# Performance work log

Measured on AMD Instinct MI355X. Metric: run time of the kernel, lower is better.

The kernel has to match this reference:

```python
import jax, jax.numpy as jnp
import numpy as np
import math

B, S, D, H = 4, 1024, 1024, 16
DK = D // H


def setup_inputs() -> dict:
    key = jax.random.key(0)
    ks = jax.random.split(key, 12)
    inp = {
        "q": jax.random.normal(ks[0], (B, S, D), jnp.float32),
        "k": jax.random.normal(ks[1], (B, S, D), jnp.float32),
        "v": jax.random.normal(ks[2], (B, S, D), jnp.float32),
        # causal mask, broadcast over batch (0 = masked)
        "mask": jnp.broadcast_to(jnp.tril(jnp.ones((S, S), jnp.int32)), (B, S, S)),
    }
    sc = 1.0 / math.sqrt(D)
    # torch nn.Linear convention: y = x @ W.T + b, W:[out,in]
    inp["Wq"] = jax.random.normal(ks[3], (D, D), jnp.float32) * sc
    inp["bq"] = jnp.zeros((D,), jnp.float32)
    inp["Wk"] = jax.random.normal(ks[4], (D, D), jnp.float32) * sc
    inp["bk"] = jnp.zeros((D,), jnp.float32)
    inp["Wv"] = jax.random.normal(ks[5], (D, D), jnp.float32) * sc
    inp["bv"] = jnp.zeros((D,), jnp.float32)
    inp["Wo"] = jax.random.normal(ks[6], (D, D), jnp.float32) * sc
    inp["bo"] = jnp.zeros((D,), jnp.float32)
    return inp


def _mha(q, k, v, mask, Wq, bq, Wk, bk, Wv, bv, Wo, bo):
    def split_heads(x):  # [B,S,D] -> [B,H,S,DK]
        return x.reshape(B, S, H, DK).transpose(0, 2, 1, 3)

    qh = split_heads(q @ Wq.T + bq)
    kh = split_heads(k @ Wk.T + bk)
    vh = split_heads(v @ Wv.T + bv)

    scores = jnp.einsum("bhqd,bhkd->bhqk", qh, kh) / math.sqrt(DK)
    scores = jnp.where(mask[:, None, :, :] == 0, jnp.float32(-1e9), scores)
    weights = jax.nn.softmax(scores, axis=-1)  # dropout in eval mode -> identity
    out = jnp.einsum("bhqk,bhkd->bhqd", weights, vh)
    out = out.transpose(0, 2, 1, 3).reshape(B, S, D)
    return out @ Wo.T + bo


def reference(q, k, v, mask, Wq, bq, Wk, bk, Wv, bv, Wo, bo):
    return _mha(q, k, v, mask, Wq, bq, Wk, bk, Wv, bv, Wo, bo)
```

## Files before the change

kernel.cpp:

```cpp
#include <hip/hip_runtime.h>

typedef unsigned short u16;
typedef __bf16 bf16x8 __attribute__((ext_vector_type(8)));
typedef float floatx4 __attribute__((ext_vector_type(4)));

#define BB 4
#define SS 1024
#define DD 1024
#define HH 16
#define DKK 64
#define MM (BB*SS)

__device__ __forceinline__ u16 f2bf(float f) {
    union { float f; unsigned int u; } v; v.f = f;
    unsigned int r = v.u + 0x7fffu + ((v.u >> 16) & 1u);
    return (u16)(r >> 16);
}

__device__ __forceinline__ void async16(const u16* g, u16* l) {
    __builtin_amdgcn_global_load_lds(
        (const __attribute__((address_space(1))) void*)g,
        (__attribute__((address_space(3))) void*)l,
        16, 0, 0);
}

__global__ __launch_bounds__(256) void convert_kernel(
    const float* __restrict__ q, const float* __restrict__ k, const float* __restrict__ v,
    const float* __restrict__ Wq, const float* __restrict__ Wk, const float* __restrict__ Wv,
    const float* __restrict__ Wo,
    u16* qb, u16* kb, u16* vb, u16* Wqb, u16* Wkb, u16* Wvb, u16* Wob) {
    const int Q4 = (BB*SS*DD) / 4;
    const int W4 = (DD*DD) / 4;
    int idx = blockIdx.x * 256 + threadIdx.x;
    const float* src; u16* dst; int off;
    if (idx < Q4)            { src = q; dst = qb; off = idx; }
    else if (idx < 2*Q4)     { src = k; dst = kb; off = idx - Q4; }
    else if (idx < 3*Q4)     { src = v; dst = vb; off = idx - 2*Q4; }
    else {
        int r = idx - 3*Q4;
        int wsel = r / W4; off = r - wsel*W4;
        src = wsel==0 ? Wq : wsel==1 ? Wk : wsel==2 ? Wv : Wo;
        dst = wsel==0 ? Wqb : wsel==1 ? Wkb : wsel==2 ? Wvb : Wob;
    }
    float4 x = ((const float4*)src)[off];
    ushort4 y;
    y.x = f2bf(x.x); y.y = f2bf(x.y); y.z = f2bf(x.z); y.w = f2bf(x.w);
    ((ushort4*)dst)[off] = y;
}

__global__ __launch_bounds__(256) void qkv_gemm(
    const u16* __restrict__ qb, const u16* __restrict__ kb, const u16* __restrict__ vb,
    const u16* __restrict__ Wqb, const u16* __restrict__ Wkb, const u16* __restrict__ Wvb,
    const float* __restrict__ bq, const float* __restrict__ bk, const float* __restrict__ bv,
    u16* Qh, u16* Kh, u16* Vt) {
    const int K = DD;
    __shared__ u16 sA[128*32];
    __shared__ u16 sW[128*32];

    int flat = blockIdx.x + 24 * blockIdx.y;
    int qg  = flat >> 6;
    int rem = flat & 63;
    int nB  = rem >> 3;
    int x8  = rem & 7;
    int wmi = (qg << 3) | x8;
    int which = wmi >> 5;
    int m0 = (wmi & 31) * 128;
    int n0 = nB * 128;

    const u16* A   = which==0 ? qb  : which==1 ? kb  : vb;
    const u16* W   = which==0 ? Wqb : which==1 ? Wkb : Wvb;
    const float* bias = which==0 ? bq : which==1 ? bk : bv;
    u16* Out = which==0 ? Qh : which==1 ? Kh : Vt;
    float scale = which==0 ? 0.125f : 1.0f;

    int t = threadIdx.x;
    int w = t >> 6, l = t & 63, g = l >> 4, c = l & 15;
    int wm = w & 1, wn = w >> 1;
    int sw = (g ^ (c & 3)) * 8;

    floatx4 acc[4][4] = {};

    int srow = t >> 2;
    int sseg = (t & 3) ^ (srow & 3);
    const u16* gA0 = A + (size_t)(m0 + srow) * K + sseg*8;
    const u16* gW0 = W + (size_t)(n0 + srow) * K + sseg*8;
    u16* lA = &sA[t*8];
    u16* lW = &sW[t*8];

    for (int kk = 0; kk < K; kk += 32) {
        __syncthreads();
        async16(gA0 + kk,          lA);
        async16(gA0 + 64*K + kk,   lA + 64*32);
        async16(gW0 + kk,          lW);
        async16(gW0 + 64*K + kk,   lW + 64*32);
        __syncthreads();
        bf16x8 af[4], bf_[4];
        #pragma unroll
        for (int i = 0; i < 4; i++) af[i]  = *(const bf16x8*)&sA[(wm*64 + i*16 + c)*32 + sw];
        #pragma unroll
        for (int j = 0; j < 4; j++) bf_[j] = *(const bf16x8*)&sW[(wn*64 + j*16 + c)*32 + sw];
        #pragma unroll
        for (int i = 0; i < 4; i++)
            #pragma unroll
            for (int j = 0; j < 4; j++)
                acc[i][j] = __builtin_amdgcn_mfma_f32_16x16x32_bf16(af[i], bf_[j], acc[i][j], 0, 0, 0);
    }

    #pragma unroll
    for (int j = 0; j < 4; j++) {
        int col = n0 + wn*64 + j*16 + c;
        float bb = bias[col];
        int h = col >> 6, dk = col & 63;
        #pragma unroll
        for (int i = 0; i < 4; i++) {
            #pragma unroll
            for (int r = 0; r < 4; r++) {
                int row = m0 + wm*64 + i*16 + g*4 + r;
                int b = row >> 10, s = row & 1023;
                float vv = (acc[i][j][r] + bb) * scale;
                u16 bits = f2bf(vv);
                if (which == 2) {
                    Out[((size_t)((b*HH + h)*DKK + dk))*SS + s] = bits;
                } else {
                    Out[((size_t)(b*HH + h)*SS + s)*DKK + dk] = bits;
                }
            }
        }
    }
}

__global__ __launch_bounds__(256) void attn_kernel(
    const u16* __restrict__ Qh, const u16* __restrict__ Kh, const u16* __restrict__ Vt,
    u16* __restrict__ attnO) {
    __shared__ u16 sQ[64*64];
    __shared__ u16 sK[2][64*64];
    __shared__ u16 sVt[2][64*64];
    __shared__ u16 sP[64*72];

    int bh = blockIdx.y;
    const u16* Qp  = Qh + (size_t)bh * SS * DKK;
    const u16* Kp  = Kh + (size_t)bh * SS * DKK;
    const u16* Vtp = Vt + (size_t)bh * DKK * SS;
    int b = bh >> 4, h = bh & 15;

    int t = threadIdx.x, w = t >> 6, l = t & 63, g = l >> 4, c = l & 15;
    int wq = w * 16;
    int cx = c & 7;

    bf16x8 bones;
    {
        __bf16 one = (__bf16)1.0f, zero = (__bf16)0.0f;
        __bf16 val = (c == 0) ? one : zero;
        #pragma unroll
        for (int j = 0; j < 8; j++) bones[j] = val;
    }

    int qi0 = t, qi1 = t + 256;
    int r0 = qi0 >> 3, s0 = (qi0 & 7) ^ (r0 & 7);
    int r1 = qi1 >> 3, s1 = (qi1 & 7) ^ (r1 & 7);

    #pragma unroll
    for (int phase = 0; phase < 2; phase++) {
        int qt = phase == 0 ? (15 - (int)blockIdx.x) : (int)blockIdx.x;
        int q0 = qt * 64;

        __syncthreads();
        async16(&Qp[(q0 + r0)*DKK + s0*8], &sQ[qi0*8]);
        async16(&Qp[(q0 + r1)*DKK + s1*8], &sQ[qi1*8]);
        async16(&Kp[(r0)*DKK + s0*8],      &sK[0][qi0*8]);
        async16(&Kp[(r1)*DKK + s1*8],      &sK[0][qi1*8]);
        async16(&Vtp[r0*SS + s0*8],        &sVt[0][qi0*8]);
        async16(&Vtp[r1*SS + s1*8],        &sVt[0][qi1*8]);

        floatx4 o[4] = {};
        floatx4 ol = {};
        int cur = 0;

        for (int k0 = 0; k0 <= q0; k0 += 64) {
            __syncthreads();
            int kn = k0 + 64;
            if (kn <= q0) {
                async16(&Kp[(kn + r0)*DKK + s0*8], &sK[cur^1][qi0*8]);
                async16(&Kp[(kn + r1)*DKK + s1*8], &sK[cur^1][qi1*8]);
                async16(&Vtp[r0*SS + kn + s0*8],   &sVt[cur^1][qi0*8]);
                async16(&Vtp[r1*SS + kn + s1*8],   &sVt[cur^1][qi1*8]);
            }

            floatx4 sc_[4] = {};
            #pragma unroll
            for (int ks = 0; ks < 2; ks++) {
                int so = ((ks*4 + g) ^ cx) * 8;
                bf16x8 aq = *(const bf16x8*)&sQ[(wq + c)*64 + so];
                #pragma unroll
                for (int nt = 0; nt < 4; nt++) {
                    bf16x8 bk_ = *(const bf16x8*)&sK[cur][(nt*16 + c)*64 + so];
                    sc_[nt] = __builtin_amdgcn_mfma_f32_16x16x32_bf16(aq, bk_, sc_[nt], 0, 0, 0);
                }
            }

            if (k0 == q0) {
                #pragma unroll
                for (int nt = 0; nt < 4; nt++)
                    #pragma unroll
                    for (int r = 0; r < 4; r++) {
                        int qg = wq + g*4 + r;
                        int kg = nt*16 + c;
                        if (kg > qg) sc_[nt][r] = -1e30f;
                    }
            }

            #pragma unroll
            for (int r = 0; r < 4; r++) {
                int prow = (wq + g*4 + r)*72;
                #pragma unroll
                for (int nt = 0; nt < 4; nt++) {
                    float p = __expf(sc_[nt][r]);
                    sP[prow + nt*16 + c] = f2bf(p);
                }
            }

            #pragma unroll
            for (int ks = 0; ks < 2; ks++) {
                int so = ((ks*4 + g) ^ cx) * 8;
                bf16x8 ap = *(const bf16x8*)&sP[(wq + c)*72 + ks*32 + g*8];
                #pragma unroll
                for (int nt = 0; nt < 4; nt++) {
                    bf16x8 bv_ = *(const bf16x8*)&sVt[cur][(nt*16 + c)*64 + so];
                    o[nt] = __builtin_amdgcn_mfma_f32_16x16x32_bf16(ap, bv_, o[nt], 0, 0, 0);
                }
                ol = __builtin_amdgcn_mfma_f32_16x16x32_bf16(ap, bones, ol, 0, 0, 0);
            }
            cur ^= 1;
        }

        #pragma unroll
        for (int r = 0; r < 4; r++) {
            float lv = __shfl(ol[r], l & 48);
            float inv = 1.0f / lv;
            int row = q0 + wq + g*4 + r;
            #pragma unroll
            for (int nt = 0; nt < 4; nt++) {
                int dcol = h*64 + nt*16 + c;
                attnO[((size_t)b*SS + row)*DD + dcol] = f2bf(o[nt][r] * inv);
            }
        }
    }
}

__global__ __launch_bounds__(256) void out_gemm(
    const u16* __restrict__ A, const u16* __restrict__ W,
    const float* __restrict__ bo, float* __restrict__ out) {
    const int K = DD;
    __shared__ u16 sA[64*32];
    __shared__ u16 sW[128*32];
    int n0 = blockIdx.x * 128;
    int m0 = blockIdx.y * 64;

    int t = threadIdx.x;
    int w = t >> 6, l = t & 63, g = l >> 4, c = l & 15;
    int wm = w & 1, wn = w >> 1;
    int sw = (g ^ (c & 3)) * 8;

    floatx4 acc[2][4] = {};

    int srow = t >> 2;
    int sseg = (t & 3) ^ (srow & 3);
    const u16* gA0 = A + (size_t)(m0 + srow) * K + sseg*8;
    const u16* gW0 = W + (size_t)(n0 + srow) * K + sseg*8;
    u16* lA = &sA[t*8];
    u16* lW = &sW[t*8];

    for (int kk = 0; kk < K; kk += 32) {
        __syncthreads();
        async16(gA0 + kk,        lA);
        async16(gW0 + kk,        lW);
        async16(gW0 + 64*K + kk, lW + 64*32);
        __syncthreads();
        bf16x8 af[2], bf_[4];
        #pragma unroll
        for (int i = 0; i < 2; i++) af[i]  = *(const bf16x8*)&sA[(wm*32 + i*16 + c)*32 + sw];
        #pragma unroll
        for (int j = 0; j < 4; j++) bf_[j] = *(const bf16x8*)&sW[(wn*64 + j*16 + c)*32 + sw];
        #pragma unroll
        for (int i = 0; i < 2; i++)
            #pragma unroll
            for (int j = 0; j < 4; j++)
                acc[i][j] = __builtin_amdgcn_mfma_f32_16x16x32_bf16(af[i], bf_[j], acc[i][j], 0, 0, 0);
    }

    #pragma unroll
    for (int j = 0; j < 4; j++) {
        int col = n0 + wn*64 + j*16 + c;
        float bb = bo[col];
        #pragma unroll
        for (int i = 0; i < 2; i++) {
            #pragma unroll
            for (int r = 0; r < 4; r++) {
                int row = m0 + wm*32 + i*16 + g*4 + r;
                out[(size_t)row*DD + col] = acc[i][j][r] + bb;
            }
        }
    }
}

extern "C" void kernel_launch(void* const* d_in, const int* in_sizes, int n_in,
                              void* d_out, int out_size, void* d_ws, size_t ws_size,
                              hipStream_t stream) {
    const float* q    = (const float*)d_in[0];
    const float* k    = (const float*)d_in[1];
    const float* v    = (const float*)d_in[2];
    const float* Wq   = (const float*)d_in[4];
    const float* bq   = (const float*)d_in[5];
    const float* Wk   = (const float*)d_in[6];
    const float* bk   = (const float*)d_in[7];
    const float* Wv   = (const float*)d_in[8];
    const float* bv   = (const float*)d_in[9];
    const float* Wo   = (const float*)d_in[10];
    const float* bo   = (const float*)d_in[11];
    float* out = (float*)d_out;

    char* ws = (char*)d_ws;
    const size_t MB = 1024*1024;
    u16* qb   = (u16*)(ws + 0*MB);
    u16* kb   = (u16*)(ws + 8*MB);
    u16* vb   = (u16*)(ws + 16*MB);
    u16* Wqb  = (u16*)(ws + 24*MB);
    u16* Wkb  = (u16*)(ws + 26*MB);
    u16* Wvb  = (u16*)(ws + 28*MB);
    u16* Wob  = (u16*)(ws + 30*MB);
    u16* Qh   = (u16*)(ws + 32*MB);
    u16* Kh   = (u16*)(ws + 40*MB);
    u16* Vt   = (u16*)(ws + 48*MB);
    u16* attn = (u16*)(ws + 56*MB);

    convert_kernel<<<16384, 256, 0, stream>>>(q, k, v, Wq, Wk, Wv, Wo,
                                              qb, kb, vb, Wqb, Wkb, Wvb, Wob);
    qkv_gemm<<<dim3(24, 32), 256, 0, stream>>>(qb, kb, vb, Wqb, Wkb, Wvb,
                                               bq, bk, bv, Qh, Kh, Vt);
    attn_kernel<<<dim3(8, 64), 256, 0, stream>>>(Qh, Kh, Vt, attn);
    out_gemm<<<dim3(8, 64), 256, 0, stream>>>(attn, Wob, bo, out);
}
```

Before: 217.3 us.

## Double-buffer LDS tiles in QKV and output GEMMs and refine swizzle

Both projection GEMMs now keep two LDS buffers and issue the async global-to-LDS loads for the next K-slice before the MFMAs on the current slice. This drops one barrier per iteration and lets the global loads overlap with the matrix math. The LDS swizzle also XORs in one more row bit, to spread the fragment reads over more banks. In exchange, LDS use per block doubles, which may lower occupancy, and the end-of-iteration barrier still waits for the prefetch to finish.

```diff
diff --git a/kernel.cpp b/kernel.cpp
--- a/kernel.cpp
+++ b/kernel.cpp
@@ -54,8 +54,8 @@
     const float* __restrict__ bq, const float* __restrict__ bk, const float* __restrict__ bv,
     u16* Qh, u16* Kh, u16* Vt) {
     const int K = DD;
-    __shared__ u16 sA[128*32];
-    __shared__ u16 sW[128*32];
+    __shared__ u16 sA[2][128*32];
+    __shared__ u16 sW[2][128*32];
 
     int flat = blockIdx.x + 24 * blockIdx.y;
     int qg  = flat >> 6;
@@ -76,34 +76,42 @@
     int t = threadIdx.x;
     int w = t >> 6, l = t & 63, g = l >> 4, c = l & 15;
     int wm = w & 1, wn = w >> 1;
-    int sw = (g ^ (c & 3)) * 8;
+    int sw = (g ^ (c & 3) ^ ((c >> 2) & 1)) * 8;
 
     floatx4 acc[4][4] = {};
 
     int srow = t >> 2;
-    int sseg = (t & 3) ^ (srow & 3);
+    int sseg = (t & 3) ^ (srow & 3) ^ ((srow >> 2) & 1);
     const u16* gA0 = A + (size_t)(m0 + srow) * K + sseg*8;
     const u16* gW0 = W + (size_t)(n0 + srow) * K + sseg*8;
-    u16* lA = &sA[t*8];
-    u16* lW = &sW[t*8];
-
+
+    async16(gA0,          &sA[0][t*8]);
+    async16(gA0 + 64*K,   &sA[0][64*32 + t*8]);
+    async16(gW0,          &sW[0][t*8]);
+    async16(gW0 + 64*K,   &sW[0][64*32 + t*8]);
+    __syncthreads();
+
+    int cur = 0;
     for (int kk = 0; kk < K; kk += 32) {
-        __syncthreads();
-        async16(gA0 + kk,          lA);
-        async16(gA0 + 64*K + kk,   lA + 64*32);
-        async16(gW0 + kk,          lW);
-        async16(gW0 + 64*K + kk,   lW + 64*32);
-        __syncthreads();
+        int nxt = kk + 32;
+        if (nxt < K) {
+            async16(gA0 + nxt,        &sA[cur^1][t*8]);
+            async16(gA0 + 64*K + nxt, &sA[cur^1][64*32 + t*8]);
+            async16(gW0 + nxt,        &sW[cur^1][t*8]);
+            async16(gW0 + 64*K + nxt, &sW[cur^1][64*32 + t*8]);
+        }
         bf16x8 af[4], bf_[4];
         #pragma unroll
-        for (int i = 0; i < 4; i++) af[i]  = *(const bf16x8*)&sA[(wm*64 + i*16 + c)*32 + sw];
-        #pragma unroll
-        for (int j = 0; j < 4; j++) bf_[j] = *(const bf16x8*)&sW[(wn*64 + j*16 + c)*32 + sw];
+        for (int i = 0; i < 4; i++) af[i]  = *(const bf16x8*)&sA[cur][(wm*64 + i*16 + c)*32 + sw];
+        #pragma unroll
+        for (int j = 0; j < 4; j++) bf_[j] = *(const bf16x8*)&sW[cur][(wn*64 + j*16 + c)*32 + sw];
         #pragma unroll
         for (int i = 0; i < 4; i++)
             #pragma unroll
             for (int j = 0; j < 4; j++)
                 acc[i][j] = __builtin_amdgcn_mfma_f32_16x16x32_bf16(af[i], bf_[j], acc[i][j], 0, 0, 0);
+        __syncthreads();
+        cur ^= 1;
     }
 
     #pragma unroll
@@ -251,41 +259,48 @@
     const u16* __restrict__ A, const u16* __restrict__ W,
     const float* __restrict__ bo, float* __restrict__ out) {
     const int K = DD;
-    __shared__ u16 sA[64*32];
-    __shared__ u16 sW[128*32];
+    __shared__ u16 sA[2][64*32];
+    __shared__ u16 sW[2][128*32];
     int n0 = blockIdx.x * 128;
     int m0 = blockIdx.y * 64;
 
     int t = threadIdx.x;
     int w = t >> 6, l = t & 63, g = l >> 4, c = l & 15;
     int wm = w & 1, wn = w >> 1;
-    int sw = (g ^ (c & 3)) * 8;
+    int sw = (g ^ (c & 3) ^ ((c >> 2) & 1)) * 8;
 
     floatx4 acc[2][4] = {};
 
     int srow = t >> 2;
-    int sseg = (t & 3) ^ (srow & 3);
+    int sseg = (t & 3) ^ (srow & 3) ^ ((srow >> 2) & 1);
     const u16* gA0 = A + (size_t)(m0 + srow) * K + sseg*8;
     const u16* gW0 = W + (size_t)(n0 + srow) * K + sseg*8;
-    u16* lA = &sA[t*8];
-    u16* lW = &sW[t*8];
-
+
+    async16(gA0,          &sA[0][t*8]);
+    async16(gW0,          &sW[0][t*8]);
+    async16(gW0 + 64*K,   &sW[0][64*32 + t*8]);
+    __syncthreads();
+
+    int cur = 0;
     for (int kk = 0; kk < K; kk += 32) {
-        __syncthreads();
-        async16(gA0 + kk,        lA);
-        async16(gW0 + kk,        lW);
-        async16(gW0 + 64*K + kk, lW + 64*32);
-        __syncthreads();
+        int nxt = kk + 32;
+        if (nxt < K) {
+            async16(gA0 + nxt,        &sA[cur^1][t*8]);
+            async16(gW0 + nxt,        &sW[cur^1][t*8]);
+            async16(gW0 + 64*K + nxt, &sW[cur^1][64*32 + t*8]);
+        }
         bf16x8 af[2], bf_[4];
         #pragma unroll
-        for (int i = 0; i < 2; i++) af[i]  = *(const bf16x8*)&sA[(wm*32 + i*16 + c)*32 + sw];
-        #pragma unroll
-        for (int j = 0; j < 4; j++) bf_[j] = *(const bf16x8*)&sW[(wn*64 + j*16 + c)*32 + sw];
+        for (int i = 0; i < 2; i++) af[i]  = *(const bf16x8*)&sA[cur][(wm*32 + i*16 + c)*32 + sw];
+        #pragma unroll
+        for (int j = 0; j < 4; j++) bf_[j] = *(const bf16x8*)&sW[cur][(wn*64 + j*16 + c)*32 + sw];
         #pragma unroll
         for (int i = 0; i < 2; i++)
             #pragma unroll
             for (int j = 0; j < 4; j++)
                 acc[i][j] = __builtin_amdgcn_mfma_f32_16x16x32_bf16(af[i], bf_[j], acc[i][j], 0, 0, 0);
+        __syncthreads();
+        cur ^= 1;
     }
 
     #pragma unroll
```

After: 226.4 us. 4.2% more time.

## Fuse fp32-to-bf16 activation conversion into QKV GEMM tile loads

Applied to the files above, without the earlier changes.

Stops converting the q/k/v activations to bf16 in a separate pass and has the QKV GEMM load fp32 tiles straight into LDS, converting to bf16 when building MFMA fragments. The separate pass read 48MB of fp32 and wrote 24MB of bf16 that the GEMM then read back, so this removes that round trip; only the weight conversion remains as its own kernel. In exchange the GEMM moves twice the bytes per A tile, uses more LDS, and does the conversion in the inner loop, repeated across every N-block that reuses the same rows.

```diff
diff --git a/kernel.cpp b/kernel.cpp
--- a/kernel.cpp
+++ b/kernel.cpp
@@ -17,7 +17,7 @@
     return (u16)(r >> 16);
 }
 
-__device__ __forceinline__ void async16(const u16* g, u16* l) {
+__device__ __forceinline__ void async16(const void* g, void* l) {
     __builtin_amdgcn_global_load_lds(
         (const __attribute__((address_space(1))) void*)g,
         (__attribute__((address_space(3))) void*)l,
@@ -25,23 +25,15 @@
 }
 
 __global__ __launch_bounds__(256) void convert_kernel(
-    const float* __restrict__ q, const float* __restrict__ k, const float* __restrict__ v,
     const float* __restrict__ Wq, const float* __restrict__ Wk, const float* __restrict__ Wv,
     const float* __restrict__ Wo,
-    u16* qb, u16* kb, u16* vb, u16* Wqb, u16* Wkb, u16* Wvb, u16* Wob) {
-    const int Q4 = (BB*SS*DD) / 4;
+    u16* Wqb, u16* Wkb, u16* Wvb, u16* Wob) {
     const int W4 = (DD*DD) / 4;
     int idx = blockIdx.x * 256 + threadIdx.x;
-    const float* src; u16* dst; int off;
-    if (idx < Q4)            { src = q; dst = qb; off = idx; }
-    else if (idx < 2*Q4)     { src = k; dst = kb; off = idx - Q4; }
-    else if (idx < 3*Q4)     { src = v; dst = vb; off = idx - 2*Q4; }
-    else {
-        int r = idx - 3*Q4;
-        int wsel = r / W4; off = r - wsel*W4;
-        src = wsel==0 ? Wq : wsel==1 ? Wk : wsel==2 ? Wv : Wo;
-        dst = wsel==0 ? Wqb : wsel==1 ? Wkb : wsel==2 ? Wvb : Wob;
-    }
+    int wsel = idx / W4;
+    int off  = idx - wsel*W4;
+    const float* src = wsel==0 ? Wq : wsel==1 ? Wk : wsel==2 ? Wv : Wo;
+    u16*         dst = wsel==0 ? Wqb : wsel==1 ? Wkb : wsel==2 ? Wvb : Wob;
     float4 x = ((const float4*)src)[off];
     ushort4 y;
     y.x = f2bf(x.x); y.y = f2bf(x.y); y.z = f2bf(x.z); y.w = f2bf(x.w);
@@ -49,13 +41,13 @@
 }
 
 __global__ __launch_bounds__(256) void qkv_gemm(
-    const u16* __restrict__ qb, const u16* __restrict__ kb, const u16* __restrict__ vb,
+    const float* __restrict__ qf, const float* __restrict__ kf, const float* __restrict__ vf,
     const u16* __restrict__ Wqb, const u16* __restrict__ Wkb, const u16* __restrict__ Wvb,
     const float* __restrict__ bq, const float* __restrict__ bk, const float* __restrict__ bv,
     u16* Qh, u16* Kh, u16* Vt) {
     const int K = DD;
-    __shared__ u16 sA[128*32];
-    __shared__ u16 sW[128*32];
+    __shared__ float sAf[128*32];
+    __shared__ u16   sW[128*32];
 
     int flat = blockIdx.x + 24 * blockIdx.y;
     int qg  = flat >> 6;
@@ -67,8 +59,8 @@
     int m0 = (wmi & 31) * 128;
     int n0 = nB * 128;
 
-    const u16* A   = which==0 ? qb  : which==1 ? kb  : vb;
-    const u16* W   = which==0 ? Wqb : which==1 ? Wkb : Wvb;
+    const float* A   = which==0 ? qf  : which==1 ? kf  : vf;
+    const u16*   W   = which==0 ? Wqb : which==1 ? Wkb : Wvb;
     const float* bias = which==0 ? bq : which==1 ? bk : bv;
     u16* Out = which==0 ? Qh : which==1 ? Kh : Vt;
     float scale = which==0 ? 0.125f : 1.0f;
@@ -77,26 +69,42 @@
     int w = t >> 6, l = t & 63, g = l >> 4, c = l & 15;
     int wm = w & 1, wn = w >> 1;
     int sw = (g ^ (c & 3)) * 8;
+    int s7 = c & 7;
 
     floatx4 acc[4][4] = {};
 
+    const float* gAf[4]; float* lAf[4];
+    #pragma unroll
+    for (int qld = 0; qld < 4; qld++) {
+        int id = qld*256 + t;
+        int row = id >> 3, pq = id & 7;
+        int lq = pq ^ (row & 7);
+        gAf[qld] = A + (size_t)(m0 + row) * K + lq*4;
+        lAf[qld] = &sAf[id*4];
+    }
     int srow = t >> 2;
     int sseg = (t & 3) ^ (srow & 3);
-    const u16* gA0 = A + (size_t)(m0 + srow) * K + sseg*8;
     const u16* gW0 = W + (size_t)(n0 + srow) * K + sseg*8;
-    u16* lA = &sA[t*8];
     u16* lW = &sW[t*8];
 
     for (int kk = 0; kk < K; kk += 32) {
         __syncthreads();
-        async16(gA0 + kk,          lA);
-        async16(gA0 + 64*K + kk,   lA + 64*32);
-        async16(gW0 + kk,          lW);
-        async16(gW0 + 64*K + kk,   lW + 64*32);
+        #pragma unroll
+        for (int qld = 0; qld < 4; qld++) async16(gAf[qld] + kk, lAf[qld]);
+        async16(gW0 + kk,        lW);
+        async16(gW0 + 64*K + kk, lW + 64*32);
         __syncthreads();
         bf16x8 af[4], bf_[4];
         #pragma unroll
-        for (int i = 0; i < 4; i++) af[i]  = *(const bf16x8*)&sA[(wm*64 + i*16 + c)*32 + sw];
+        for (int i = 0; i < 4; i++) {
+            int row = wm*64 + i*16 + c;
+            const float4 lo = *(const float4*)&sAf[row*32 + (((2*g)  ) ^ s7)*4];
+            const float4 hi = *(const float4*)&sAf[row*32 + (((2*g)|1) ^ s7)*4];
+            af[i][0] = (__bf16)lo.x; af[i][1] = (__bf16)lo.y;
+            af[i][2] = (__bf16)lo.z; af[i][3] = (__bf16)lo.w;
+            af[i][4] = (__bf16)hi.x; af[i][5] = (__bf16)hi.y;
+            af[i][6] = (__bf16)hi.z; af[i][7] = (__bf16)hi.w;
+        }
         #pragma unroll
         for (int j = 0; j < 4; j++) bf_[j] = *(const bf16x8*)&sW[(wn*64 + j*16 + c)*32 + sw];
         #pragma unroll
@@ -321,9 +329,6 @@
 
     char* ws = (char*)d_ws;
     const size_t MB = 1024*1024;
-    u16* qb   = (u16*)(ws + 0*MB);
-    u16* kb   = (u16*)(ws + 8*MB);
-    u16* vb   = (u16*)(ws + 16*MB);
     u16* Wqb  = (u16*)(ws + 24*MB);
     u16* Wkb  = (u16*)(ws + 26*MB);
     u16* Wvb  = (u16*)(ws + 28*MB);
@@ -333,9 +338,8 @@
     u16* Vt   = (u16*)(ws + 48*MB);
     u16* attn = (u16*)(ws + 56*MB);
 
-    convert_kernel<<<16384, 256, 0, stream>>>(q, k, v, Wq, Wk, Wv, Wo,
-                                              qb, kb, vb, Wqb, Wkb, Wvb, Wob);
-    qkv_gemm<<<dim3(24, 32), 256, 0, stream>>>(qb, kb, vb, Wqb, Wkb, Wvb,
+    convert_kernel<<<4096, 256, 0, stream>>>(Wq, Wk, Wv, Wo, Wqb, Wkb, Wvb, Wob);
+    qkv_gemm<<<dim3(24, 32), 256, 0, stream>>>(q, k, v, Wqb, Wkb, Wvb,
                                                bq, bk, bv, Qh, Kh, Vt);
     attn_kernel<<<dim3(8, 64), 256, 0, stream>>>(Qh, Kh, Vt, attn);
     out_gemm<<<dim3(8, 64), 256, 0, stream>>>(attn, Wob, bo, out);
```

Result: slower. 233.6 us (+7.5%).

## Rewrite QKV GEMM as 256x256 tile, 8-wave, double-buffered ping-pong pipeline

Applied to the files above, without the earlier changes.

The QKV projection GEMM moves from 128x128 tiles with 4 waves and a single LDS buffer to 256x256 tiles with 8 waves, launched as 192 workgroups. K-chunks of 64 are double-buffered in LDS, and async global-to-LDS loads are interleaved with MFMA phases using explicit vmcnt waits, barriers, sched_barrier and setprio. The V-transpose epilogue also writes packed ushort4 stores. The aim is to hide global load latency and raise arithmetic intensity, at the cost of heavier register and LDS use and only 192 blocks, which may underfill the CUs.

```diff
diff --git a/kernel.cpp b/kernel.cpp
--- a/kernel.cpp
+++ b/kernel.cpp
@@ -17,7 +17,7 @@
     return (u16)(r >> 16);
 }
 
-__device__ __forceinline__ void async16(const u16* g, u16* l) {
+__device__ __forceinline__ void async16(const void* g, void* l) {
     __builtin_amdgcn_global_load_lds(
         (const __attribute__((address_space(1))) void*)g,
         (__attribute__((address_space(3))) void*)l,
@@ -48,81 +48,119 @@
     ((ushort4*)dst)[off] = y;
 }
 
-__global__ __launch_bounds__(256) void qkv_gemm(
+__global__ __launch_bounds__(512, 2) void qkv_gemm(
     const u16* __restrict__ qb, const u16* __restrict__ kb, const u16* __restrict__ vb,
     const u16* __restrict__ Wqb, const u16* __restrict__ Wkb, const u16* __restrict__ Wvb,
     const float* __restrict__ bq, const float* __restrict__ bk, const float* __restrict__ bv,
     u16* Qh, u16* Kh, u16* Vt) {
-    const int K = DD;
-    __shared__ u16 sA[128*32];
-    __shared__ u16 sW[128*32];
-
-    int flat = blockIdx.x + 24 * blockIdx.y;
-    int qg  = flat >> 6;
-    int rem = flat & 63;
-    int nB  = rem >> 3;
-    int x8  = rem & 7;
-    int wmi = (qg << 3) | x8;
-    int which = wmi >> 5;
-    int m0 = (wmi & 31) * 128;
-    int n0 = nB * 128;
-
-    const u16* A   = which==0 ? qb  : which==1 ? kb  : vb;
-    const u16* W   = which==0 ? Wqb : which==1 ? Wkb : Wvb;
+    __shared__ u16 sA[2][2][8192];
+    __shared__ u16 sB[2][2][8192];
+
+    int flat = blockIdx.x;
+    int x8 = flat & 7;
+    int j_ = flat >> 3;
+    int wmi = x8*6 + (j_ >> 2);
+    int nB  = j_ & 3;
+    int which = wmi >> 4;
+    int m0 = (wmi & 15) * 256;
+    int n0 = nB * 256;
+
+    const u16* Ag = which==0 ? qb  : which==1 ? kb  : vb;
+    const u16* Wg = which==0 ? Wqb : which==1 ? Wkb : Wvb;
     const float* bias = which==0 ? bq : which==1 ? bk : bv;
     u16* Out = which==0 ? Qh : which==1 ? Kh : Vt;
     float scale = which==0 ? 0.125f : 1.0f;
 
     int t = threadIdx.x;
     int w = t >> 6, l = t & 63, g = l >> 4, c = l & 15;
-    int wm = w & 1, wn = w >> 1;
-    int sw = (g ^ (c & 3)) * 8;
-
-    floatx4 acc[4][4] = {};
+    int wm = w >> 2, wn = w & 3;
+    int qo = (g ^ (c & 3)) * 8;
 
     int srow = t >> 2;
-    int sseg = (t & 3) ^ (srow & 3);
-    const u16* gA0 = A + (size_t)(m0 + srow) * K + sseg*8;
-    const u16* gW0 = W + (size_t)(n0 + srow) * K + sseg*8;
-    u16* lA = &sA[t*8];
-    u16* lW = &sW[t*8];
-
-    for (int kk = 0; kk < K; kk += 32) {
-        __syncthreads();
-        async16(gA0 + kk,          lA);
-        async16(gA0 + 64*K + kk,   lA + 64*32);
-        async16(gW0 + kk,          lW);
-        async16(gW0 + 64*K + kk,   lW + 64*32);
-        __syncthreads();
-        bf16x8 af[4], bf_[4];
-        #pragma unroll
-        for (int i = 0; i < 4; i++) af[i]  = *(const bf16x8*)&sA[(wm*64 + i*16 + c)*32 + sw];
-        #pragma unroll
-        for (int j = 0; j < 4; j++) bf_[j] = *(const bf16x8*)&sW[(wn*64 + j*16 + c)*32 + sw];
-        #pragma unroll
-        for (int i = 0; i < 4; i++)
-            #pragma unroll
-            for (int j = 0; j < 4; j++)
-                acc[i][j] = __builtin_amdgcn_mfma_f32_16x16x32_bf16(af[i], bf_[j], acc[i][j], 0, 0, 0);
-    }
+    int lsegv = (t & 3) ^ (srow & 3);
+    const u16* srcA0 = Ag + (size_t)(m0 + srow) * 1024 + lsegv*8;
+    const u16* srcA1 = Ag + (size_t)(m0 + 128 + srow) * 1024 + lsegv*8;
+    const u16* srcB0 = Wg + (size_t)(n0 + srow) * 1024 + lsegv*8;
+    const u16* srcB1 = Wg + (size_t)(n0 + 128 + srow) * 1024 + lsegv*8;
+    int d0 = t*8, d1 = 4096 + t*8;
+
+#define STG_A(KT, KH, BUF) { int _col = (KT)*64 + (KH)*32;            \
+    async16(srcA0 + _col, &sA[BUF][KH][d0]);                          \
+    async16(srcA1 + _col, &sA[BUF][KH][d1]); }
+#define STG_B(KT, KH, BUF) { int _col = (KT)*64 + (KH)*32;            \
+    async16(srcB0 + _col, &sB[BUF][KH][d0]);                          \
+    async16(srcB1 + _col, &sB[BUF][KH][d1]); }
+
+    floatx4 acc[8][4] = {};
+
+#define PHASE(CH, KH, BUF, STAGE_STMT, VM8)                                   \
+  {                                                                           \
+    bf16x8 af[4], bfv[4];                                                     \
+    _Pragma("unroll")                                                         \
+    for (int i = 0; i < 4; i++)                                               \
+      af[i] = *(const bf16x8*)&sA[BUF][KH][(wm*128 + CH*64 + i*16 + c)*32 + qo]; \
+    _Pragma("unroll")                                                         \
+    for (int j = 0; j < 4; j++)                                               \
+      bfv[j] = *(const bf16x8*)&sB[BUF][KH][(wn*64 + j*16 + c)*32 + qo];      \
+    STAGE_STMT;                                                               \
+    if (VM8) asm volatile("s_waitcnt vmcnt(8)" ::: "memory");                 \
+    __builtin_amdgcn_s_barrier();                                             \
+    asm volatile("s_waitcnt lgkmcnt(0)" ::: "memory");                        \
+    __builtin_amdgcn_sched_barrier(0);                                        \
+    __builtin_amdgcn_s_setprio(1);                                            \
+    _Pragma("unroll")                                                         \
+    for (int i = 0; i < 4; i++)                                               \
+      _Pragma("unroll")                                                       \
+      for (int j = 0; j < 4; j++)                                             \
+        acc[CH*4+i][j] = __builtin_amdgcn_mfma_f32_16x16x32_bf16(af[i], bfv[j], acc[CH*4+i][j], 0, 0, 0); \
+    __builtin_amdgcn_s_setprio(0);                                            \
+    __builtin_amdgcn_sched_barrier(0);                                        \
+    __builtin_amdgcn_s_barrier();                                             \
+  }
+
+    STG_A(0,0,0); STG_B(0,0,0); STG_A(0,1,0); STG_B(0,1,0); STG_A(1,0,1); STG_B(1,0,1);
+    asm volatile("s_waitcnt vmcnt(8)" ::: "memory");
+    __builtin_amdgcn_s_barrier();
+
+    #pragma unroll 1
+    for (int tt = 0; tt < 8; ++tt) {
+        int t1 = 2*tt + 1;
+        int n1 = (2*tt+2 < 16) ? 2*tt+2 : 15;
+        int n2 = (2*tt+3 < 16) ? 2*tt+3 : 15;
+        PHASE(0,0,0, STG_A(t1,1,1), 0)
+        PHASE(1,0,0, STG_B(t1,1,1), 1)
+        PHASE(0,1,0, STG_A(n1,0,0), 0)
+        PHASE(1,1,0, STG_B(n1,0,0), 1)
+        PHASE(0,0,1, STG_A(n1,1,0), 0)
+        PHASE(1,0,1, STG_B(n1,1,0), 1)
+        PHASE(0,1,1, STG_A(n2,0,1), 0)
+        PHASE(1,1,1, STG_B(n2,0,1), 1)
+    }
+#undef PHASE
+#undef STG_A
+#undef STG_B
 
     #pragma unroll
-    for (int j = 0; j < 4; j++) {
-        int col = n0 + wn*64 + j*16 + c;
-        float bb = bias[col];
-        int h = col >> 6, dk = col & 63;
-        #pragma unroll
-        for (int i = 0; i < 4; i++) {
-            #pragma unroll
-            for (int r = 0; r < 4; r++) {
-                int row = m0 + wm*64 + i*16 + g*4 + r;
-                int b = row >> 10, s = row & 1023;
-                float vv = (acc[i][j][r] + bb) * scale;
-                u16 bits = f2bf(vv);
-                if (which == 2) {
-                    Out[((size_t)((b*HH + h)*DKK + dk))*SS + s] = bits;
-                } else {
-                    Out[((size_t)(b*HH + h)*SS + s)*DKK + dk] = bits;
+    for (int i2 = 0; i2 < 8; i2++) {
+        int row0 = m0 + wm*128 + i2*16 + g*4;
+        int b_ = row0 >> 10, s0_ = row0 & 1023;
+        #pragma unroll
+        for (int j = 0; j < 4; j++) {
+            int col = n0 + wn*64 + j*16 + c;
+            float bb = bias[col];
+            int h = col >> 6, dk = col & 63;
+            if (which == 2) {
+                ushort4 pk;
+                pk.x = f2bf(acc[i2][j][0] + bb);
+                pk.y = f2bf(acc[i2][j][1] + bb);
+                pk.z = f2bf(acc[i2][j][2] + bb);
+                pk.w = f2bf(acc[i2][j][3] + bb);
+                *(ushort4*)&Out[((size_t)((b_*HH + h)*DKK + dk))*SS + s0_] = pk;
+            } else {
+                #pragma unroll
+                for (int r = 0; r < 4; r++) {
+                    float vv = (acc[i2][j][r] + bb) * scale;
+                    Out[((size_t)(b_*HH + h)*SS + (s0_ + r))*DKK + dk] = f2bf(vv);
                 }
             }
         }
@@ -335,8 +373,8 @@
 
     convert_kernel<<<16384, 256, 0, stream>>>(q, k, v, Wq, Wk, Wv, Wo,
                                               qb, kb, vb, Wqb, Wkb, Wvb, Wob);
-    qkv_gemm<<<dim3(24, 32), 256, 0, stream>>>(qb, kb, vb, Wqb, Wkb, Wvb,
-                                               bq, bk, bv, Qh, Kh, Vt);
+    qkv_gemm<<<192, 512, 0, stream>>>(qb, kb, vb, Wqb, Wkb, Wvb,
+                                      bq, bk, bv, Qh, Kh, Vt);
     attn_kernel<<<dim3(8, 64), 256, 0, stream>>>(Qh, Kh, Vt, attn);
     out_gemm<<<dim3(8, 64), 256, 0, stream>>>(attn, Wob, bo, out);
 }
```

New measurement: 221.9 us. 1.02x slower.
